# Performance work log

Hardware: AMD Instinct MI355X
Metric: run time of the kernel (lower is better)

## Reference

```python
import jax, jax.numpy as jnp
import numpy as np

B = 2
C = 256
NH = 8
DH = C // NH
NL = 4
NP = 4
NLAYERS = 6
DFF = 1024
SHAPES = [(128, 128), (64, 64), (32, 32), (16, 16)]
LQ = sum(h * w for h, w in SHAPES)
STARTS = np.cumsum([0] + [h * w for h, w in SHAPES])[:-1].tolist()


def _ln(x, g, b, eps=1e-5):
    mu = jnp.mean(x, -1, keepdims=True)
    var = jnp.mean((x - mu) ** 2, -1, keepdims=True)
    return (x - mu) * jax.lax.rsqrt(var + eps) * g + b


def _ref_points():
    # centers of each cell, normalized to [0,1]; valid_ratios == 1 (masks=None path)
    pts = []
    for (h, w) in SHAPES:
        ry = (np.arange(h) + 0.5) / h
        rx = (np.arange(w) + 0.5) / w
        gy, gx = np.meshgrid(ry, rx, indexing='ij')
        pts.append(np.stack([gx.reshape(-1), gy.reshape(-1)], -1))
    return jnp.asarray(np.concatenate(pts, 0), jnp.float32)  # [LQ,2] (x,y)


def _bilinear(vf, loc, Hl, Wl):
    # vf: [B,NH,S,DH] flattened level features; loc: [B,LQ,NH,NP,2] in [0,1]
    # grid_sample semantics: bilinear, zero padding, align_corners=False
    x = loc[..., 0] * Wl - 0.5
    y = loc[..., 1] * Hl - 0.5
    x0 = jnp.floor(x)
    y0 = jnp.floor(y)
    wx = x - x0
    wy = y - y0
    out = 0.0
    for dx, dy, w in ((0, 0, (1 - wx) * (1 - wy)), (1, 0, wx * (1 - wy)),
                      (0, 1, (1 - wx) * wy), (1, 1, wx * wy)):
        xi = x0 + dx
        yi = y0 + dy
        valid = (xi >= 0) & (xi < Wl) & (yi >= 0) & (yi < Hl)
        idx = (jnp.clip(yi, 0, Hl - 1) * Wl + jnp.clip(xi, 0, Wl - 1)).astype(jnp.int32)
        idx = jnp.transpose(idx, (0, 2, 1, 3)).reshape(B, NH, -1)  # [B,NH,LQ*NP]
        g = jnp.take_along_axis(vf, idx[..., None], axis=2)        # [B,NH,LQ*NP,DH]
        wgt = jnp.transpose(w * valid, (0, 2, 1, 3)).reshape(B, NH, -1)
        out = out + g * wgt[..., None]
    return out.reshape(B, NH, LQ, NP, DH)


def _forward(src0, src1, src2, src3, pos0, pos1, pos2, pos3, level_embed,
             Woff, boff, Wattn, battn, Wval, bval, Wout, bout,
             g1, b1, Wff1, bff1, Wff2, bff2, g2, b2):
    srcs = [src0, src1, src2, src3]
    poss = [pos0, pos1, pos2, pos3]
    src = jnp.concatenate([s.reshape(B, C, -1).transpose(0, 2, 1) for s in srcs], 1)
    pos = jnp.concatenate([p.reshape(B, C, -1).transpose(0, 2, 1) + level_embed[l][None, None]
                           for l, p in enumerate(poss)], 1)
    ref = _ref_points()  # [LQ,2]
    norm_wh = jnp.asarray([[w, h] for (h, w) in SHAPES], jnp.float32)  # offset_normalizer
    x = src
    for l in range(NLAYERS):
        q = x + pos
        off = (q @ Woff[l] + boff[l]).reshape(B, LQ, NH, NL, NP, 2)
        attn = jax.nn.softmax((q @ Wattn[l] + battn[l]).reshape(B, LQ, NH, NL * NP), -1)
        attn = attn.reshape(B, LQ, NH, NL, NP)
        val = (x @ Wval[l] + bval[l]).reshape(B, LQ, NH, DH)
        loc = ref[None, :, None, None, None, :] + off / norm_wh[None, None, None, :, None, :]
        out = jnp.zeros((B, NH, LQ, DH), x.dtype)
        for lv, (h, w) in enumerate(SHAPES):
            s0 = STARTS[lv]
            vf = val[:, s0:s0 + h * w].transpose(0, 2, 1, 3)   # [B,NH,S,DH]
            samp = _bilinear(vf, loc[:, :, :, lv], h, w)       # [B,NH,LQ,NP,DH]
            a = attn[:, :, :, lv].transpose(0, 2, 1, 3)        # [B,NH,LQ,NP]
            out = out + jnp.einsum('bhqpd,bhqp->bhqd', samp, a)
        out = out.transpose(0, 2, 1, 3).reshape(B, LQ, C) @ Wout[l] + bout[l]
        x = _ln(x + out, g1[l], b1[l])
        ff = jax.nn.relu(x @ Wff1[l] + bff1[l]) @ Wff2[l] + bff2[l]
        x = _ln(x + ff, g2[l], b2[l])
    return x


def setup_inputs() -> dict:
    key = jax.random.key(0)
    ks = jax.random.split(key, 20)
    d = {}
    for i, (h, w) in enumerate(SHAPES):
        d[f'src{i}'] = jax.random.normal(ks[i], (B, C, h, w), jnp.float32)
        d[f'pos{i}'] = jax.random.normal(ks[4 + i], (B, C, h, w), jnp.float32) * 0.1
    d['level_embed'] = jax.random.normal(ks[8], (NL, C), jnp.float32)

    def lin(k, fi, fo, scale=None):
        s = scale if scale is not None else 1.0 / np.sqrt(fi)
        return jax.random.normal(k, (NLAYERS, fi, fo), jnp.float32) * s

    d['Woff'] = lin(ks[9], C, NH * NL * NP * 2, 0.01)
    d['boff'] = jax.random.uniform(ks[10], (NLAYERS, NH * NL * NP * 2), jnp.float32, -0.5, 0.5)
    d['Wattn'] = lin(ks[11], C, NH * NL * NP)
    d['battn'] = jnp.zeros((NLAYERS, NH * NL * NP), jnp.float32)
    d['Wval'] = lin(ks[12], C, C)
    d['bval'] = jnp.zeros((NLAYERS, C), jnp.float32)
    d['Wout'] = lin(ks[13], C, C)
    d['bout'] = jnp.zeros((NLAYERS, C), jnp.float32)
    d['g1'] = jnp.ones((NLAYERS, C), jnp.float32)
    d['b1'] = jnp.zeros((NLAYERS, C), jnp.float32)
    d['Wff1'] = lin(ks[14], C, DFF)
    d['bff1'] = jnp.zeros((NLAYERS, DFF), jnp.float32)
    d['Wff2'] = lin(ks[15], DFF, C)
    d['bff2'] = jnp.zeros((NLAYERS, C), jnp.float32)
    d['g2'] = jnp.ones((NLAYERS, C), jnp.float32)
    d['b2'] = jnp.zeros((NLAYERS, C), jnp.float32)
    return d


def reference(src0, src1, src2, src3, pos0, pos1, pos2, pos3, level_embed,
              Woff, boff, Wattn, battn, Wval, bval, Wout, bout,
              g1, b1, Wff1, bff1, Wff2, bff2, g2, b2):
    return _forward(src0, src1, src2, src3, pos0, pos1, pos2, pos3, level_embed,
                    Woff, boff, Wattn, battn, Wval, bval, Wout, bout,
                    g1, b1, Wff1, bff1, Wff2, bff2, g2, b2)
```

## Files before the change

### kernel.cpp

```cpp
#include <hip/hip_runtime.h>
#include <hip/hip_bf16.h>
#include <hip/hip_fp16.h>
#include <math.h>

namespace {
constexpr int B_   = 2;
constexpr int C_   = 256;
constexpr int NH_  = 8;
constexpr int DH_  = 32;
constexpr int NP_  = 4;
constexpr int DFF_ = 1024;
constexpr int LQ_  = 21760;
constexpr int M_   = B_ * LQ_;
}

typedef __bf16  bf16x8 __attribute__((ext_vector_type(8)));
typedef short   s16x8  __attribute__((ext_vector_type(8)));
typedef float   f32x4  __attribute__((ext_vector_type(4)));

static __device__ __forceinline__ unsigned short f2bf(float f) {
    return __builtin_bit_cast(unsigned short, __float2bfloat16(f));
}
static __device__ __forceinline__ float bf2f(unsigned short u) {
    return __bfloat162float(__builtin_bit_cast(__hip_bfloat16, u));
}

__global__ void k_wt(const float* __restrict__ in, __hip_bfloat16* __restrict__ out,
                     int K, int N, int outStride)
{
    __shared__ float tile[32][33];
    int n0 = blockIdx.x * 32, k0 = blockIdx.y * 32;
    const float* inl = in + (size_t)blockIdx.z * K * N;
    __hip_bfloat16* outl = out + (size_t)blockIdx.z * outStride;
    for (int i = threadIdx.y; i < 32; i += 8)
        tile[i][threadIdx.x] = inl[(size_t)(k0 + i) * N + n0 + threadIdx.x];
    __syncthreads();
    for (int i = threadIdx.y; i < 32; i += 8)
        outl[(size_t)(n0 + i) * K + k0 + threadIdx.x] = __float2bfloat16(tile[threadIdx.x][i]);
}

__global__ __launch_bounds__(256) void k_assemble2(
    const float* __restrict__ s0, const float* __restrict__ s1,
    const float* __restrict__ s2, const float* __restrict__ s3,
    const float* __restrict__ p0, const float* __restrict__ p1,
    const float* __restrict__ p2, const float* __restrict__ p3,
    const float* __restrict__ lev, float* __restrict__ x,
    __hip_bfloat16* __restrict__ xbf, __hip_bfloat16* __restrict__ posbf,
    __hip_bfloat16* __restrict__ qbf)
{
    int bid = blockIdx.x;
    int lv, rem, HW, S0;
    const float *sp, *pp;
    if (bid < 8192)       { lv = 0; rem = bid;         HW = 16384; S0 = 0;     sp = s0; pp = p0; }
    else if (bid < 10240) { lv = 1; rem = bid - 8192;  HW = 4096;  S0 = 16384; sp = s1; pp = p1; }
    else if (bid < 10752) { lv = 2; rem = bid - 10240; HW = 1024;  S0 = 20480; sp = s2; pp = p2; }
    else                  { lv = 3; rem = bid - 10752; HW = 256;   S0 = 21504; sp = s3; pp = p3; }
    int sptiles = HW >> 5;
    int spt = rem % sptiles;
    int ct  = (rem / sptiles) & 7;
    int b   = rem / (sptiles * 8);
    int sp0 = spt * 32, c0 = ct * 32;

    __shared__ float ts[32][33], tp[32][33];
    int tx = threadIdx.x & 31, ty = threadIdx.x >> 5;
#pragma unroll
    for (int i = 0; i < 4; i++) {
        int c = c0 + ty + i * 8;
        size_t si = ((size_t)(b * C_ + c)) * HW + sp0 + tx;
        ts[ty + i * 8][tx] = sp[si];
        tp[ty + i * 8][tx] = pp[si];
    }
    __syncthreads();
#pragma unroll
    for (int i = 0; i < 4; i++) {
        int s = S0 + sp0 + ty + i * 8;
        int c = c0 + tx;
        float sv = ts[tx][ty + i * 8];
        float pv = tp[tx][ty + i * 8] + lev[lv * C_ + c];
        size_t idx = ((size_t)(b * LQ_ + s)) * C_ + c;
        x[idx]     = sv;
        xbf[idx]   = __float2bfloat16(sv);
        posbf[idx] = __float2bfloat16(pv);
        qbf[idx]   = __float2bfloat16(sv + pv);
    }
}

template<bool RELU, bool BF16OUT>
__global__ __launch_bounds__(256) void k_gemm_mfma(
    const __hip_bfloat16* __restrict__ A,
    const __hip_bfloat16* __restrict__ Wt,
    const float* __restrict__ bias,
    void* __restrict__ Co,
    int M, int N, int K)
{
    __shared__ char As[128 * 128];
    __shared__ char Bs[128 * 128];
    int t = threadIdx.x, w = t >> 6, lane = t & 63;
    int m0 = blockIdx.x * 128, n0 = blockIdx.y * 128;
    int wm = w >> 1, wn = w & 1;

    f32x4 acc[4][4] = {};

    int rowoff  = lane >> 3;
    int colswz  = ((lane & 7) ^ (lane >> 3)) << 3;

    for (int kt = 0; kt < K; kt += 64) {
#pragma unroll
        for (int j = 0; j < 4; j++) {
            int rowbase = w * 32 + j * 8;
            const __hip_bfloat16* srcA = A  + (size_t)(m0 + rowbase + rowoff) * K + kt + colswz;
            const __hip_bfloat16* srcB = Wt + (size_t)(n0 + rowbase + rowoff) * K + kt + colswz;
            __builtin_amdgcn_global_load_lds(
                (const __attribute__((address_space(1))) void*)srcA,
                (__attribute__((address_space(3))) void*)(As + rowbase * 128), 16, 0, 0);
            __builtin_amdgcn_global_load_lds(
                (const __attribute__((address_space(1))) void*)srcB,
                (__attribute__((address_space(3))) void*)(Bs + rowbase * 128), 16, 0, 0);
        }
        __syncthreads();
#pragma unroll
        for (int k0 = 0; k0 < 64; k0 += 32) {
            int kb = k0 * 2 + (lane >> 4) * 16;
            bf16x8 af[4], bfr[4];
#pragma unroll
            for (int mi = 0; mi < 4; mi++) {
                int r = wm * 64 + mi * 16 + (lane & 15);
                s16x8 raw = *(const s16x8*)(As + r * 128 + (kb ^ ((r & 7) << 4)));
                af[mi] = __builtin_bit_cast(bf16x8, raw);
            }
#pragma unroll
            for (int ni = 0; ni < 4; ni++) {
                int r = wn * 64 + ni * 16 + (lane & 15);
                s16x8 raw = *(const s16x8*)(Bs + r * 128 + (kb ^ ((r & 7) << 4)));
                bfr[ni] = __builtin_bit_cast(bf16x8, raw);
            }
#pragma unroll
            for (int mi = 0; mi < 4; mi++)
#pragma unroll
                for (int ni = 0; ni < 4; ni++)
                    acc[mi][ni] = __builtin_amdgcn_mfma_f32_16x16x32_bf16(
                        af[mi], bfr[ni], acc[mi][ni], 0, 0, 0);
        }
        __syncthreads();
    }

#pragma unroll
    for (int ni = 0; ni < 4; ni++) {
        int col = n0 + wn * 64 + ni * 16 + (lane & 15);
        float bb = bias[col];
#pragma unroll
        for (int mi = 0; mi < 4; mi++) {
            int row = m0 + wm * 64 + mi * 16 + ((lane >> 4) << 2);
#pragma unroll
            for (int r = 0; r < 4; r++) {
                float v = acc[mi][ni][r] + bb;
                if (RELU) v = fmaxf(v, 0.f);
                if (BF16OUT)
                    ((__hip_bfloat16*)Co)[(size_t)(row + r) * N + col] = __float2bfloat16(v);
                else
                    ((float*)Co)[(size_t)(row + r) * N + col] = v;
            }
        }
    }
}

__global__ __launch_bounds__(256) void k_gemm_qa(
    const __hip_bfloat16* __restrict__ A,
    const __hip_bfloat16* __restrict__ Wq,
    const float* __restrict__ boff, const float* __restrict__ battn,
    __half* __restrict__ offh, float* __restrict__ attb, int M)
{
    constexpr int K = 256;
    __shared__ char As[128 * 128];
    __shared__ char Bs[128 * 128];
    int t = threadIdx.x, w = t >> 6, lane = t & 63;
    int m0 = blockIdx.x * 128, n0 = blockIdx.y * 128;
    int wm = w >> 1, wn = w & 1;

    f32x4 acc[4][4] = {};
    int rowoff  = lane >> 3;
    int colswz  = ((lane & 7) ^ (lane >> 3)) << 3;

    for (int kt = 0; kt < K; kt += 64) {
#pragma unroll
        for (int j = 0; j < 4; j++) {
            int rowbase = w * 32 + j * 8;
            const __hip_bfloat16* srcA = A  + (size_t)(m0 + rowbase + rowoff) * K + kt + colswz;
            const __hip_bfloat16* srcB = Wq + (size_t)(n0 + rowbase + rowoff) * K + kt + colswz;
            __builtin_amdgcn_global_load_lds(
                (const __attribute__((address_space(1))) void*)srcA,
                (__attribute__((address_space(3))) void*)(As + rowbase * 128), 16, 0, 0);
            __builtin_amdgcn_global_load_lds(
                (const __attribute__((address_space(1))) void*)srcB,
                (__attribute__((address_space(3))) void*)(Bs + rowbase * 128), 16, 0, 0);
        }
        __syncthreads();
#pragma unroll
        for (int k0 = 0; k0 < 64; k0 += 32) {
            int kb = k0 * 2 + (lane >> 4) * 16;
            bf16x8 af[4], bfr[4];
#pragma unroll
            for (int mi = 0; mi < 4; mi++) {
                int r = wm * 64 + mi * 16 + (lane & 15);
                s16x8 raw = *(const s16x8*)(As + r * 128 + (kb ^ ((r & 7) << 4)));
                af[mi] = __builtin_bit_cast(bf16x8, raw);
            }
#pragma unroll
            for (int ni = 0; ni < 4; ni++) {
                int r = wn * 64 + ni * 16 + (lane & 15);
                s16x8 raw = *(const s16x8*)(Bs + r * 128 + (kb ^ ((r & 7) << 4)));
                bfr[ni] = __builtin_bit_cast(bf16x8, raw);
            }
#pragma unroll
            for (int mi = 0; mi < 4; mi++)
#pragma unroll
                for (int ni = 0; ni < 4; ni++)
                    acc[mi][ni] = __builtin_amdgcn_mfma_f32_16x16x32_bf16(
                        af[mi], bfr[ni], acc[mi][ni], 0, 0, 0);
        }
        __syncthreads();
    }

    if (blockIdx.y == 2) {
#pragma unroll
        for (int ni = 0; ni < 4; ni++) {
            int col = wn * 64 + ni * 16 + (lane & 15);
            float bb = battn[col];
#pragma unroll
            for (int mi = 0; mi < 4; mi++) {
                int row = m0 + wm * 64 + mi * 16 + ((lane >> 4) << 2);
#pragma unroll
                for (int r = 0; r < 4; r++)
                    attb[(size_t)(row + r) * 128 + col] = acc[mi][ni][r] + bb;
            }
        }
    } else {
#pragma unroll
        for (int ni = 0; ni < 4; ni++) {
            int col = n0 + wn * 64 + ni * 16 + (lane & 15);
            float bb = boff[col];
#pragma unroll
            for (int mi = 0; mi < 4; mi++) {
                int row = m0 + wm * 64 + mi * 16 + ((lane >> 4) << 2);
#pragma unroll
                for (int r = 0; r < 4; r++)
                    offh[(size_t)(row + r) * 256 + col] = __float2half(acc[mi][ni][r] + bb);
            }
        }
    }
}

template<bool WRITE_Q>
__global__ __launch_bounds__(256) void k_gemm_ln(
    const __hip_bfloat16* __restrict__ A,
    const __hip_bfloat16* __restrict__ Wt,
    const float* __restrict__ bias,
    float* __restrict__ xio,
    __hip_bfloat16* __restrict__ xbf,
    const float* __restrict__ g, const float* __restrict__ beta,
    const __hip_bfloat16* __restrict__ posb,
    __hip_bfloat16* __restrict__ qout,
    int M, int K)
{
    __shared__ char As[64 * 128];
    __shared__ char Bs[256 * 128];
    __shared__ float sred1[64][4];
    __shared__ float sred2[64][4];

    int t = threadIdx.x, w = t >> 6, lane = t & 63;
    int m0 = blockIdx.x * 64;

    f32x4 acc[4][4] = {};

    int rowoff  = lane >> 3;
    int colswz  = ((lane & 7) ^ rowoff) << 3;

    for (int kt = 0; kt < K; kt += 64) {
#pragma unroll
        for (int j = 0; j < 2; j++) {
            int rowbase = w * 8 + j * 32;
            const __hip_bfloat16* srcA = A + (size_t)(m0 + rowbase + rowoff) * K + kt + colswz;
            __builtin_amdgcn_global_load_lds(
                (const __attribute__((address_space(1))) void*)srcA,
                (__attribute__((address_space(3))) void*)(As + rowbase * 128), 16, 0, 0);
        }
#pragma unroll
        for (int j = 0; j < 8; j++) {
            int rowbase = w * 8 + j * 32;
            const __hip_bfloat16* srcB = Wt + (size_t)(rowbase + rowoff) * K + kt + colswz;
            __builtin_amdgcn_global_load_lds(
                (const __attribute__((address_space(1))) void*)srcB,
                (__attribute__((address_space(3))) void*)(Bs + rowbase * 128), 16, 0, 0);
        }
        __syncthreads();
#pragma unroll
        for (int k0 = 0; k0 < 64; k0 += 32) {
            int kb = k0 * 2 + (lane >> 4) * 16;
            bf16x8 af[4], bfr[4];
#pragma unroll
            for (int mi = 0; mi < 4; mi++) {
                int r = mi * 16 + (lane & 15);
                s16x8 raw = *(const s16x8*)(As + r * 128 + (kb ^ ((r & 7) << 4)));
                af[mi] = __builtin_bit_cast(bf16x8, raw);
            }
#pragma unroll
            for (int ni = 0; ni < 4; ni++) {
                int r = w * 64 + ni * 16 + (lane & 15);
                s16x8 raw = *(const s16x8*)(Bs + r * 128 + (kb ^ ((r & 7) << 4)));
                bfr[ni] = __builtin_bit_cast(bf16x8, raw);
            }
#pragma unroll
            for (int mi = 0; mi < 4; mi++)
#pragma unroll
                for (int ni = 0; ni < 4; ni++)
                    acc[mi][ni] = __builtin_amdgcn_mfma_f32_16x16x32_bf16(
                        af[mi], bfr[ni], acc[mi][ni], 0, 0, 0);
        }
        __syncthreads();
    }

    int cl = lane & 15;
    int rg = (lane >> 4) << 2;
    float bcol[4], gcol[4], btcol[4];
#pragma unroll
    for (int ni = 0; ni < 4; ni++) {
        int col = w * 64 + ni * 16 + cl;
        bcol[ni]  = bias[col];
        gcol[ni]  = g[col];
        btcol[ni] = beta[col];
    }

#pragma unroll
    for (int mi = 0; mi < 4; mi++)
#pragma unroll
    for (int r = 0; r < 4; r++) {
        int lr  = mi * 16 + rg + r;
        int row = m0 + lr;
        float s = 0.f;
#pragma unroll
        for (int ni = 0; ni < 4; ni++) {
            int col = w * 64 + ni * 16 + cl;
            float v = acc[mi][ni][r] + bcol[ni] + xio[(size_t)row * 256 + col];
            acc[mi][ni][r] = v;
            s += v;
        }
        s += __shfl_xor(s, 1); s += __shfl_xor(s, 2);
        s += __shfl_xor(s, 4); s += __shfl_xor(s, 8);
        if (cl == 0) sred1[lr][w] = s;
    }
    __syncthreads();

    float mu[4][4];
#pragma unroll
    for (int mi = 0; mi < 4; mi++)
#pragma unroll
    for (int r = 0; r < 4; r++) {
        int lr = mi * 16 + rg + r;
        mu[mi][r] = (sred1[lr][0] + sred1[lr][1] + sred1[lr][2] + sred1[lr][3]) * (1.f / 256.f);
        float s2 = 0.f;
#pragma unroll
        for (int ni = 0; ni < 4; ni++) {
            float d = acc[mi][ni][r] - mu[mi][r];
            s2 += d * d;
        }
        s2 += __shfl_xor(s2, 1); s2 += __shfl_xor(s2, 2);
        s2 += __shfl_xor(s2, 4); s2 += __shfl_xor(s2, 8);
        if (cl == 0) sred2[lr][w] = s2;
    }
    __syncthreads();

#pragma unroll
    for (int mi = 0; mi < 4; mi++)
#pragma unroll
    for (int r = 0; r < 4; r++) {
        int lr  = mi * 16 + rg + r;
        int row = m0 + lr;
        float var = (sred2[lr][0] + sred2[lr][1] + sred2[lr][2] + sred2[lr][3]) * (1.f / 256.f);
        float rstd = rsqrtf(var + 1e-5f);
#pragma unroll
        for (int ni = 0; ni < 4; ni++) {
            int col = w * 64 + ni * 16 + cl;
            size_t idx = (size_t)row * 256 + col;
            float o = (acc[mi][ni][r] - mu[mi][r]) * rstd * gcol[ni] + btcol[ni];
            xio[idx] = o;
            xbf[idx] = __float2bfloat16(o);
            if (WRITE_Q)
                qout[idx] = __float2bfloat16(o + bf2f(__builtin_bit_cast(unsigned short, posb[idx])));
        }
    }
}

__global__ __launch_bounds__(256) void k_sample3(const __hip_bfloat16* __restrict__ val,
                                                 const __half* __restrict__ offh,
                                                 const float* __restrict__ logits,
                                                 __hip_bfloat16* __restrict__ out)
{
    __shared__ int2 sIW[4 * 32 * 16];

    int t  = threadIdx.x;
    int qb = blockIdx.x;

#pragma unroll
    for (int it = 0; it < 2; it++) {
        int item = t + it * 256;
        int qi = item >> 7;
        int pt = item & 127;
        int bs = qb * 4 + qi;
        int b  = bs / LQ_;
        int s  = bs % LQ_;
        int h  = pt >> 4, lv = (pt >> 2) & 3;

        float lg = logits[(size_t)bs * 128 + pt];
        float mx = lg;
#pragma unroll
        for (int m = 1; m < 16; m <<= 1) mx = fmaxf(mx, __shfl_xor(mx, m));
        float ex = __expf(lg - mx);
        float sm = ex;
#pragma unroll
        for (int m = 1; m < 16; m <<= 1) sm += __shfl_xor(sm, m);
        float aw = ex / sm;

        int p0, Wq;
        if (s < 16384)      { p0 = s;         Wq = 128; }
        else if (s < 20480) { p0 = s - 16384; Wq = 64;  }
        else if (s < 21504) { p0 = s - 20480; Wq = 32;  }
        else                { p0 = s - 21504; Wq = 16;  }
        float invWq = 1.f / (float)Wq;
        float refx = ((p0 % Wq) + 0.5f) * invWq;
        float refy = ((p0 / Wq) + 0.5f) * invWq;

        int W  = 128 >> lv;
        int S0 = (65536 - (65536 >> (2 * lv))) / 3;
        float fW = (float)W;

        __half2 o2 = ((const __half2*)(offh + (size_t)bs * 256))[pt];
        float ox = __low2float(o2), oy = __high2float(o2);
        float xx = refx * fW + ox - 0.5f;
        float yy = refy * fW + oy - 0.5f;
        float x0f = floorf(xx), y0f = floorf(yy);
        float wx = xx - x0f, wy = yy - y0f;
        int x0 = (int)x0f, y0 = (int)y0f;
        int x1 = x0 + 1, y1 = y0 + 1;
        bool vx0 = (x0 >= 0) & (x0 < W), vx1 = (x1 >= 0) & (x1 < W);
        bool vy0 = (y0 >= 0) & (y0 < W), vy1 = (y1 >= 0) & (y1 < W);
        int cx0 = min(max(x0, 0), W - 1), cx1 = min(max(x1, 0), W - 1);
        int cy0 = min(max(y0, 0), W - 1), cy1 = min(max(y1, 0), W - 1);

        int rowbase = (b * LQ_ + S0) * C_ + h * DH_;
        int g  = item >> 4;
        int pj = pt & 15;
        int i00 = (rowbase + (cy0 * W + cx0) * C_) * 2;
        int i10 = (rowbase + (cy0 * W + cx1) * C_) * 2;
        int i01 = (rowbase + (cy1 * W + cx0) * C_) * 2;
        int i11 = (rowbase + (cy1 * W + cx1) * C_) * 2;
        float w00 = aw * (1.f - wx) * (1.f - wy) * ((vx0 & vy0) ? 1.f : 0.f);
        float w10 = aw * wx * (1.f - wy) * ((vx1 & vy0) ? 1.f : 0.f);
        float w01 = aw * (1.f - wx) * wy * ((vx0 & vy1) ? 1.f : 0.f);
        float w11 = aw * wx * wy * ((vx1 & vy1) ? 1.f : 0.f);
        sIW[(0 * 32 + g) * 16 + pj] = make_int2(i00, __float_as_int(w00));
        sIW[(1 * 32 + g) * 16 + pj] = make_int2(i10, __float_as_int(w10));
        sIW[(2 * 32 + g) * 16 + pj] = make_int2(i01, __float_as_int(w01));
        sIW[(3 * 32 + g) * 16 + pj] = make_int2(i11, __float_as_int(w11));
    }
    __syncthreads();

    {
        int g  = t >> 3;
        int dq = t & 7;
        int bs = qb * 4 + (g >> 3);
        int h  = g & 7;
        int dbyte = dq * 8;

        const char* vbase = (const char*)val;
        float a0 = 0.f, a1 = 0.f, a2 = 0.f, a3 = 0.f;
#pragma unroll
        for (int j = 0; j < 16; j++) {
#pragma unroll
            for (int k = 0; k < 4; k++) {
                int2 iw = sIW[(k * 32 + g) * 16 + j];
                float w = __int_as_float(iw.y);
                uint2 u = *(const uint2*)(vbase + iw.x + dbyte);
                a0 = fmaf(w, __builtin_bit_cast(float, u.x << 16), a0);
                a1 = fmaf(w, __builtin_bit_cast(float, u.x & 0xffff0000u), a1);
                a2 = fmaf(w, __builtin_bit_cast(float, u.y << 16), a2);
                a3 = fmaf(w, __builtin_bit_cast(float, u.y & 0xffff0000u), a3);
            }
        }
        uint2 o;
        o.x = (unsigned)f2bf(a0) | ((unsigned)f2bf(a1) << 16);
        o.y = (unsigned)f2bf(a2) | ((unsigned)f2bf(a3) << 16);
        *(uint2*)((char*)out + (size_t)bs * 512 + h * 64 + dbyte) = o;
    }
}

extern "C" void kernel_launch(void* const* d_in, const int* in_sizes, int n_in,
                              void* d_out, int out_size, void* d_ws, size_t ws_size,
                              hipStream_t stream)
{
    const float* src_[4] = {(const float*)d_in[0], (const float*)d_in[2],
                            (const float*)d_in[4], (const float*)d_in[6]};
    const float* pos_[4] = {(const float*)d_in[1], (const float*)d_in[3],
                            (const float*)d_in[5], (const float*)d_in[7]};
    const float* lev   = (const float*)d_in[8];
    const float* Woff  = (const float*)d_in[9];
    const float* boff  = (const float*)d_in[10];
    const float* Wattn = (const float*)d_in[11];
    const float* battn = (const float*)d_in[12];
    const float* Wval  = (const float*)d_in[13];
    const float* bval  = (const float*)d_in[14];
    const float* Wout  = (const float*)d_in[15];
    const float* bout  = (const float*)d_in[16];
    const float* g1    = (const float*)d_in[17];
    const float* b1    = (const float*)d_in[18];
    const float* Wff1  = (const float*)d_in[19];
    const float* bff1  = (const float*)d_in[20];
    const float* Wff2  = (const float*)d_in[21];
    const float* bff2  = (const float*)d_in[22];
    const float* g2    = (const float*)d_in[23];
    const float* b2    = (const float*)d_in[24];

    float* x = (float*)d_out;
    size_t MC = (size_t)M_ * C_;

    __hip_bfloat16* pos_bf = (__hip_bfloat16*)d_ws;
    __hip_bfloat16* q_bf   = pos_bf + MC;
    __hip_bfloat16* x_bf   = q_bf + MC;
    __half* offh           = (__half*)(x_bf + MC);
    float*  attb           = (float*)(offh + MC);
    __hip_bfloat16* val_bf = (__hip_bfloat16*)(attb + (size_t)M_ * 128);
    __hip_bfloat16* pad_bf = val_bf + MC;
    __hip_bfloat16* ffh_bf = (__hip_bfloat16*)offh;
    __hip_bfloat16* wbf    = pad_bf + MC;

    __hip_bfloat16* wq    = wbf;
    __hip_bfloat16* wvalt = wq    + 6 * 98304;
    __hip_bfloat16* woutt = wvalt + 6 * 65536;
    __hip_bfloat16* wff1t = woutt + 6 * 65536;
    __hip_bfloat16* wff2t = wff1t + 6 * 262144;

    dim3 blk(256);
    dim3 tblk(32, 8);

    k_wt<<<dim3(8, 8, 6),  tblk, 0, stream>>>(Woff,  wq,               256, 256,  98304);
    k_wt<<<dim3(4, 8, 6),  tblk, 0, stream>>>(Wattn, wq + 256 * 256,   256, 128,  98304);
    k_wt<<<dim3(8, 8, 6),  tblk, 0, stream>>>(Wval,  wvalt,            256, 256,  65536);
    k_wt<<<dim3(8, 8, 6),  tblk, 0, stream>>>(Wout,  woutt,            256, 256,  65536);
    k_wt<<<dim3(32, 8, 6), tblk, 0, stream>>>(Wff1,  wff1t,            256, 1024, 262144);
    k_wt<<<dim3(8, 32, 6), tblk, 0, stream>>>(Wff2,  wff2t,            1024, 256, 262144);

    k_assemble2<<<10880, blk, 0, stream>>>(
        src_[0], src_[1], src_[2], src_[3],
        pos_[0], pos_[1], pos_[2], pos_[3], lev, x, x_bf, pos_bf, q_bf);

    for (int l = 0; l < 6; l++) {
        k_gemm_qa<<<dim3(M_ / 128, 3), blk, 0, stream>>>(
            q_bf, wq + (size_t)l * 98304, boff + l * 256, battn + l * 128,
            offh, attb, M_);

        k_gemm_mfma<false, true><<<dim3(M_ / 128, 2), blk, 0, stream>>>(
            x_bf, wvalt + (size_t)l * 65536, bval + l * 256, val_bf, M_, 256, C_);

        k_sample3<<<M_ / 4, blk, 0, stream>>>(val_bf, offh, attb, q_bf);

        k_gemm_ln<false><<<M_ / 64, blk, 0, stream>>>(
            q_bf, woutt + (size_t)l * 65536, bout + l * 256,
            x, x_bf, g1 + l * 256, b1 + l * 256,
            nullptr, nullptr, M_, C_);

        k_gemm_mfma<true, true><<<dim3(M_ / 128, 8), blk, 0, stream>>>(
            x_bf, wff1t + (size_t)l * 262144, bff1 + l * DFF_, ffh_bf, M_, DFF_, C_);

        if (l < 5)
            k_gemm_ln<true><<<M_ / 64, blk, 0, stream>>>(
                ffh_bf, wff2t + (size_t)l * 262144, bff2 + l * C_,
                x, x_bf, g2 + l * 256, b2 + l * 256,
                pos_bf, q_bf, M_, DFF_);
        else
            k_gemm_ln<false><<<M_ / 64, blk, 0, stream>>>(
                ffh_bf, wff2t + (size_t)l * 262144, bff2 + l * C_,
                x, x_bf, g2 + l * 256, b2 + l * 256,
                nullptr, nullptr, M_, DFF_);
    }
}
```

Before: 2.042 ms.

## Double-buffer LDS and widen row tile in fused GEMM+LayerNorm kernel

The GEMM+residual+LayerNorm kernel now uses 512 threads covering 128 rows, with eight waves in a 2x4 grid, so each block of B (weight) tiles is shared by twice as many rows. It also double-buffers the A and B LDS tiles, issuing the next k-tile's global-to-LDS loads before the MFMA work on the current tile. This is meant to overlap memory latency with compute and halve weight reloads per row. The cost is roughly 96KB of LDS per block and half as many blocks, which lowers occupancy and grid parallelism.

```diff
diff --git a/kernel.cpp b/kernel.cpp
--- a/kernel.cpp
+++ b/kernel.cpp
@@ -251,7 +251,7 @@
 }
 
 template<bool WRITE_Q>
-__global__ __launch_bounds__(256) void k_gemm_ln(
+__global__ __launch_bounds__(512) void k_gemm_ln(
     const __hip_bfloat16* __restrict__ A,
     const __hip_bfloat16* __restrict__ Wt,
     const float* __restrict__ bias,
@@ -262,51 +262,63 @@
     __hip_bfloat16* __restrict__ qout,
     int M, int K)
 {
-    __shared__ char As[64 * 128];
-    __shared__ char Bs[256 * 128];
-    __shared__ float sred1[64][4];
-    __shared__ float sred2[64][4];
+    __shared__ char As[2][128 * 128];
+    __shared__ char Bs[2][256 * 128];
+    __shared__ float sred1[128][4];
+    __shared__ float sred2[128][4];
 
     int t = threadIdx.x, w = t >> 6, lane = t & 63;
-    int m0 = blockIdx.x * 64;
+    int m0 = blockIdx.x * 128;
+    int wm = w >> 2, wn = w & 3;
 
     f32x4 acc[4][4] = {};
 
     int rowoff  = lane >> 3;
     int colswz  = ((lane & 7) ^ rowoff) << 3;
 
-    for (int kt = 0; kt < K; kt += 64) {
+    auto STAGE = [&](char* Ab, char* Bb, int kt) {
 #pragma unroll
         for (int j = 0; j < 2; j++) {
-            int rowbase = w * 8 + j * 32;
+            int rowbase = w * 16 + j * 8;
             const __hip_bfloat16* srcA = A + (size_t)(m0 + rowbase + rowoff) * K + kt + colswz;
             __builtin_amdgcn_global_load_lds(
                 (const __attribute__((address_space(1))) void*)srcA,
-                (__attribute__((address_space(3))) void*)(As + rowbase * 128), 16, 0, 0);
-        }
-#pragma unroll
-        for (int j = 0; j < 8; j++) {
-            int rowbase = w * 8 + j * 32;
+                (__attribute__((address_space(3))) void*)(Ab + rowbase * 128), 16, 0, 0);
+        }
+#pragma unroll
+        for (int j = 0; j < 4; j++) {
+            int rowbase = w * 32 + j * 8;
             const __hip_bfloat16* srcB = Wt + (size_t)(rowbase + rowoff) * K + kt + colswz;
             __builtin_amdgcn_global_load_lds(
                 (const __attribute__((address_space(1))) void*)srcB,
-                (__attribute__((address_space(3))) void*)(Bs + rowbase * 128), 16, 0, 0);
-        }
-        __syncthreads();
+                (__attribute__((address_space(3))) void*)(Bb + rowbase * 128), 16, 0, 0);
+        }
+    };
+
+    STAGE(As[0], Bs[0], 0);
+    asm volatile("s_waitcnt vmcnt(0)" ::: "memory");
+    __builtin_amdgcn_s_barrier();
+
+    const int nt = K >> 6;
+    int cur = 0;
+    for (int tt = 0; tt < nt; ++tt) {
+        if (tt + 1 < nt) STAGE(As[cur ^ 1], Bs[cur ^ 1], (tt + 1) << 6);
+        const char* Ab = As[cur];
+        const char* Bb = Bs[cur];
 #pragma unroll
         for (int k0 = 0; k0 < 64; k0 += 32) {
             int kb = k0 * 2 + (lane >> 4) * 16;
             bf16x8 af[4], bfr[4];
 #pragma unroll
             for (int mi = 0; mi < 4; mi++) {
-                int r = mi * 16 + (lane & 15);
-                s16x8 raw = *(const s16x8*)(As + r * 128 + (kb ^ ((r & 7) << 4)));
+                int r = wm * 64 + mi * 16 + (lane & 15);
+                s16x8 raw = *(const s16x8*)(Ab + r * 128 + (kb ^ ((r & 7) << 4)));
                 af[mi] = __builtin_bit_cast(bf16x8, raw);
             }
 #pragma unroll
             for (int ni = 0; ni < 4; ni++) {
-                int r = w * 64 + ni * 16 + (lane & 15);
-                s16x8 raw = *(const s16x8*)(Bs + r * 128 + (kb ^ ((r & 7) << 4)));
+                int r = wn * 64 + ni * 16 + (lane & 15);
+                s16x8 raw = *(const s16x8*)(Bb + r * 128 + (kb ^ ((r & 7) << 4)));
                 bfr[ni] = __builtin_bit_cast(bf16x8, raw);
             }
 #pragma unroll
@@ -316,7 +328,9 @@
                     acc[mi][ni] = __builtin_amdgcn_mfma_f32_16x16x32_bf16(
                         af[mi], bfr[ni], acc[mi][ni], 0, 0, 0);
         }
-        __syncthreads();
+        asm volatile("s_waitcnt vmcnt(0)" ::: "memory");
+        __builtin_amdgcn_s_barrier();
+        cur ^= 1;
     }
 
     int cl = lane & 15;
@@ -324,7 +338,7 @@
     float bcol[4], gcol[4], btcol[4];
 #pragma unroll
     for (int ni = 0; ni < 4; ni++) {
-        int col = w * 64 + ni * 16 + cl;
+        int col = wn * 64 + ni * 16 + cl;
         bcol[ni]  = bias[col];
         gcol[ni]  = g[col];
         btcol[ni] = beta[col];
@@ -334,19 +348,19 @@
     for (int mi = 0; mi < 4; mi++)
 #pragma unroll
     for (int r = 0; r < 4; r++) {
-        int lr  = mi * 16 + rg + r;
+        int lr  = wm * 64 + mi * 16 + rg + r;
         int row = m0 + lr;
         float s = 0.f;
 #pragma unroll
         for (int ni = 0; ni < 4; ni++) {
-            int col = w * 64 + ni * 16 + cl;
+            int col = wn * 64 + ni * 16 + cl;
             float v = acc[mi][ni][r] + bcol[ni] + xio[(size_t)row * 256 + col];
             acc[mi][ni][r] = v;
             s += v;
         }
         s += __shfl_xor(s, 1); s += __shfl_xor(s, 2);
         s += __shfl_xor(s, 4); s += __shfl_xor(s, 8);
-        if (cl == 0) sred1[lr][w] = s;
+        if (cl == 0) sred1[lr][wn] = s;
     }
     __syncthreads();
 
@@ -355,7 +369,7 @@
     for (int mi = 0; mi < 4; mi++)
 #pragma unroll
     for (int r = 0; r < 4; r++) {
-        int lr = mi * 16 + rg + r;
+        int lr = wm * 64 + mi * 16 + rg + r;
         mu[mi][r] = (sred1[lr][0] + sred1[lr][1] + sred1[lr][2] + sred1[lr][3]) * (1.f / 256.f);
         float s2 = 0.f;
 #pragma unroll
@@ -365,7 +379,7 @@
         }
         s2 += __shfl_xor(s2, 1); s2 += __shfl_xor(s2, 2);
         s2 += __shfl_xor(s2, 4); s2 += __shfl_xor(s2, 8);
-        if (cl == 0) sred2[lr][w] = s2;
+        if (cl == 0) sred2[lr][wn] = s2;
     }
     __syncthreads();
 
@@ -373,13 +387,13 @@
     for (int mi = 0; mi < 4; mi++)
 #pragma unroll
     for (int r = 0; r < 4; r++) {
-        int lr  = mi * 16 + rg + r;
+        int lr  = wm * 64 + mi * 16 + rg + r;
         int row = m0 + lr;
         float var = (sred2[lr][0] + sred2[lr][1] + sred2[lr][2] + sred2[lr][3]) * (1.f / 256.f);
         float rstd = rsqrtf(var + 1e-5f);
 #pragma unroll
         for (int ni = 0; ni < 4; ni++) {
-            int col = w * 64 + ni * 16 + cl;
+            int col = wn * 64 + ni * 16 + cl;
             size_t idx = (size_t)row * 256 + col;
             float o = (acc[mi][ni][r] - mu[mi][r]) * rstd * gcol[ni] + btcol[ni];
             xio[idx] = o;
@@ -562,7 +576,7 @@
 
         k_sample3<<<M_ / 4, blk, 0, stream>>>(val_bf, offh, attb, q_bf);
 
-        k_gemm_ln<false><<<M_ / 64, blk, 0, stream>>>(
+        k_gemm_ln<false><<<M_ / 128, 512, 0, stream>>>(
             q_bf, woutt + (size_t)l * 65536, bout + l * 256,
             x, x_bf, g1 + l * 256, b1 + l * 256,
             nullptr, nullptr, M_, C_);
@@ -571,12 +585,12 @@
             x_bf, wff1t + (size_t)l * 262144, bff1 + l * DFF_, ffh_bf, M_, DFF_, C_);
 
         if (l < 5)
-            k_gemm_ln<true><<<M_ / 64, blk, 0, stream>>>(
+            k_gemm_ln<true><<<M_ / 128, 512, 0, stream>>>(
                 ffh_bf, wff2t + (size_t)l * 262144, bff2 + l * C_,
                 x, x_bf, g2 + l * 256, b2 + l * 256,
                 pos_bf, q_bf, M_, DFF_);
         else
-            k_gemm_ln<false><<<M_ / 64, blk, 0, stream>>>(
+            k_gemm_ln<false><<<M_ / 128, 512, 0, stream>>>(
                 ffh_bf, wff2t + (size_t)l * 262144, bff2 + l * C_,
                 x, x_bf, g2 + l * 256, b2 + l * 256,
                 nullptr, nullptr, M_, DFF_);
```

After: 1.918 ms. 6.1% less time.
